# Kernel tuning notes

Measured on AMD Instinct MI355X. Metric: run time of the kernel, lower is better.

The kernel has to match this reference:

```python
import jax, jax.numpy as jnp
import numpy as np

NEG_SLOPE = 0.2
N_NODES = 50000


def _gat_layer(x, src, dst, invalid, W, al, ar, b):
    # x: [N, Fin]; src/dst: [E] (self-loops appended); invalid: [E] bool
    N = x.shape[0]
    H, F = al.shape
    z = (x @ W).reshape(N, H, F)                       # [N,H,F]
    el = jnp.sum(z * al[None], axis=-1)                # [N,H]
    er = jnp.sum(z * ar[None], axis=-1)                # [N,H]
    e = el[src] + er[dst]                              # [E,H]
    e = jnp.where(e > 0, e, NEG_SLOPE * e)             # LeakyReLU(0.2)
    e = jnp.where(invalid[:, None], -jnp.inf, e)       # removed self-loop edges
    # edge softmax per destination node (every node has a self-loop -> max finite)
    m = jax.ops.segment_max(e, dst, num_segments=N)    # [N,H]
    ex = jnp.exp(e - m[dst])
    ex = jnp.where(invalid[:, None], 0.0, ex)
    s = jax.ops.segment_sum(ex, dst, num_segments=N)   # [N,H]
    alpha = ex / s[dst]                                # [E,H]
    msg = z[src] * alpha[:, :, None]                   # [E,H,F]
    out = jax.ops.segment_sum(msg, dst, num_segments=N)  # [N,H,F]
    out = out + b.reshape(1, H, F)
    return jax.nn.elu(out)


def _with_self_loops(src, dst):
    N = N_NODES
    loop = jnp.arange(N, dtype=src.dtype)
    invalid = jnp.concatenate([src == dst, jnp.zeros(N, dtype=bool)])
    return jnp.concatenate([src, loop]), jnp.concatenate([dst, loop]), invalid


def setup_inputs() -> dict:
    key = jax.random.key(0)
    ks = jax.random.split(key, 12)
    N, Fin, H0, F0, H1, C = N_NODES, 256, 4, 32, 1, 40
    E = 800000
    sc = lambda k, shp, fan: jax.random.normal(k, shp, jnp.float32) * (1.0 / np.sqrt(fan))
    return {
        "x": jax.random.normal(ks[0], (N, Fin), jnp.float32),
        "src": jax.random.randint(ks[1], (E,), 0, N, jnp.int32),
        "dst": jax.random.randint(ks[2], (E,), 0, N, jnp.int32),
        "W0": sc(ks[3], (Fin, H0 * F0), Fin),
        "al0": sc(ks[4], (H0, F0), F0),
        "ar0": sc(ks[5], (H0, F0), F0),
        "b0": jnp.zeros((H0 * F0,), jnp.float32),
        "W1": sc(ks[6], (H0 * F0, H1 * C), H0 * F0),
        "al1": sc(ks[7], (H1, C), C),
        "ar1": sc(ks[8], (H1, C), C),
        "b1": jnp.zeros((C,), jnp.float32),
    }


def reference(x, src, dst, W0, al0, ar0, b0, W1, al1, ar1, b1):
    s, d, invalid = _with_self_loops(src, dst)
    h = _gat_layer(x, s, d, invalid, W0, al0, ar0, b0)   # [N,4,32]
    h = h.reshape(h.shape[0], -1)                        # flatten(1) -> [N,128]
    h = _gat_layer(h, s, d, invalid, W1, al1, ar1, b1)   # [N,1,40]
    return h.mean(axis=1)                                # mean over heads -> [N,40]
```

## Files before the change

kernel.cpp:

```cpp
#include <hip/hip_runtime.h>
#include <stdint.h>

#define NN 50000
#define EE 800000
#define CAP 48
#define NXCD 8
#define NPX 6250
#define EPB 2048
#define NCHUNK 391

typedef __bf16 bf16x8 __attribute__((ext_vector_type(8)));
typedef float  f32x4  __attribute__((ext_vector_type(4)));

__device__ __forceinline__ float bflo(unsigned int w){ union{unsigned int i;float f;}c; c.i=w<<16; return c.f; }
__device__ __forceinline__ float bfhi(unsigned int w){ union{unsigned int i;float f;}c; c.i=w&0xFFFF0000u; return c.f; }
__device__ __forceinline__ float bfs(unsigned short u){ union{unsigned int i;float f;}c; c.i=((unsigned int)u)<<16; return c.f; }
__device__ __forceinline__ bf16x8 bf8_zero(){
  bf16x8 v;
  #pragma unroll
  for (int j=0;j<8;++j) v[j]=(__bf16)0.f;
  return v;
}

__global__ __launch_bounds__(256) void k_prepW0(const float* __restrict__ W0,
                                                __bf16* __restrict__ Wg){
  int tg = blockIdx.x*256 + threadIdx.x;
  if (tg >= 4096) return;
  int k8 = tg >> 7, n = tg & 127;
  bf16x8 v;
  #pragma unroll
  for (int j=0;j<8;++j) v[j] = (__bf16)W0[(k8*8+j)*128 + n];
  *(bf16x8*)(Wg + ((size_t)(k8*128 + n))*8) = v;
}

__global__ __launch_bounds__(256) void k_gemm0(const float* __restrict__ x,
    const __bf16* __restrict__ Wg, const float* __restrict__ al0, const float* __restrict__ ar0,
    __bf16* __restrict__ z0b, float* __restrict__ el0, float* __restrict__ er0,
    int* __restrict__ cursor, int* __restrict__ csrv){
  const int tid = threadIdx.x;
  const int wv = tid >> 6, ln = tid & 63, q = ln >> 4, mr = ln & 15;
  const int nhalf = wv & 1, mhalf = wv >> 1;
  const int m0w = blockIdx.x*64 + mhalf*32;
  const int n0w = nhalf*64;
  f32x4 acc[2][4];
  #pragma unroll
  for (int mt=0;mt<2;++mt)
    #pragma unroll
    for (int nt=0;nt<4;++nt) acc[mt][nt] = (f32x4){0.f,0.f,0.f,0.f};
  const bool av0 = (m0w + mr) < NN;
  const bool av1 = (m0w + 16 + mr) < NN;
  const float* xr0 = x + (size_t)(m0w + mr)*256;
  const float* xr1 = x + (size_t)(m0w + 16 + mr)*256;
  #pragma unroll
  for (int kc=0;kc<8;++kc){
    int ko = kc*32 + q*8;
    bf16x8 a0 = bf8_zero(), a1 = bf8_zero();
    if (av0){
      float4 p = *(const float4*)(xr0 + ko);
      float4 p2 = *(const float4*)(xr0 + ko + 4);
      a0[0]=(__bf16)p.x; a0[1]=(__bf16)p.y; a0[2]=(__bf16)p.z; a0[3]=(__bf16)p.w;
      a0[4]=(__bf16)p2.x; a0[5]=(__bf16)p2.y; a0[6]=(__bf16)p2.z; a0[7]=(__bf16)p2.w;
    }
    if (av1){
      float4 p = *(const float4*)(xr1 + ko);
      float4 p2 = *(const float4*)(xr1 + ko + 4);
      a1[0]=(__bf16)p.x; a1[1]=(__bf16)p.y; a1[2]=(__bf16)p.z; a1[3]=(__bf16)p.w;
      a1[4]=(__bf16)p2.x; a1[5]=(__bf16)p2.y; a1[6]=(__bf16)p2.z; a1[7]=(__bf16)p2.w;
    }
    const __bf16* wb = Wg + ((size_t)((kc*4+q)*128 + n0w + mr))*8;
    #pragma unroll
    for (int nt=0;nt<4;++nt){
      bf16x8 bf = *(const bf16x8*)(wb + (size_t)nt*16*8);
      acc[0][nt] = __builtin_amdgcn_mfma_f32_16x16x32_bf16(a0, bf, acc[0][nt], 0,0,0);
      acc[1][nt] = __builtin_amdgcn_mfma_f32_16x16x32_bf16(a1, bf, acc[1][nt], 0,0,0);
    }
  }
  float alv[4], arv[4];
  #pragma unroll
  for (int nt=0;nt<4;++nt){ int c = n0w + nt*16 + mr; alv[nt]=al0[c]; arv[nt]=ar0[c]; }
  #pragma unroll
  for (int mt=0;mt<2;++mt){
    #pragma unroll
    for (int r=0;r<4;++r){
      int grow = m0w + mt*16 + q*4 + r;
      if (grow < NN){
        #pragma unroll
        for (int nt=0;nt<4;++nt)
          z0b[(size_t)grow*128 + n0w + nt*16 + mr] = (__bf16)acc[mt][nt][r];
      }
      float pl0 = acc[mt][0][r]*alv[0] + acc[mt][1][r]*alv[1];
      float pr0 = acc[mt][0][r]*arv[0] + acc[mt][1][r]*arv[1];
      float pl1 = acc[mt][2][r]*alv[2] + acc[mt][3][r]*alv[3];
      float pr1 = acc[mt][2][r]*arv[2] + acc[mt][3][r]*arv[3];
      #pragma unroll
      for (int off=1; off<16; off<<=1){
        pl0 += __shfl_xor(pl0, off, 16); pr0 += __shfl_xor(pr0, off, 16);
        pl1 += __shfl_xor(pl1, off, 16); pr1 += __shfl_xor(pr1, off, 16);
      }
      if (mr==0 && grow<NN){
        el0[grow*4 + 2*nhalf]   = pl0; er0[grow*4 + 2*nhalf]   = pr0;
        el0[grow*4 + 2*nhalf+1] = pl1; er0[grow*4 + 2*nhalf+1] = pr1;
        if (nhalf==0){ csrv[(size_t)grow*CAP] = grow; cursor[grow] = 1; }
      }
    }
  }
}

__global__ __launch_bounds__(256) void k_scatter(const int* __restrict__ src,
    const int* __restrict__ dst, int* __restrict__ cursor, int* __restrict__ csrv){
  const int xcd = blockIdx.x & 7;
  const int chunk = blockIdx.x >> 3;
  const int lo = xcd*NPX, hi = lo + NPX;
  int e = chunk*EPB + threadIdx.x;
  #pragma unroll
  for (int it=0; it<EPB/256; ++it, e += 256){
    if (e < EE){
      int d = dst[e];
      if (d >= lo && d < hi){
        int s = src[e];
        unsigned int inv = (s==d) ? 0x80000000u : 0u;
        int pos = atomicAdd(&cursor[d], 1);
        csrv[(size_t)d*CAP + pos] = (int)((unsigned int)s | inv);
      }
    }
  }
}

__global__ __launch_bounds__(256) void k_wedge0(const int* __restrict__ csrv,
    const int* __restrict__ cursor, const float* __restrict__ el0,
    const float* __restrict__ er0, unsigned short* __restrict__ wt){
  int slot = blockIdx.x*256 + threadIdx.x;
  int node = slot / CAP;
  int si = slot - node*CAP;
  if (si >= cursor[node]) return;
  int v = csrv[slot];
  int u = v & 0x7FFFFFFF;
  float4 ls = *(const float4*)(el0 + (size_t)u*4);
  float4 rd = *(const float4*)(er0 + (size_t)node*4);
  float e0=ls.x+rd.x; e0 = e0>0.f?e0:0.2f*e0;
  float e1=ls.y+rd.y; e1 = e1>0.f?e1:0.2f*e1;
  float e2=ls.z+rd.z; e2 = e2>0.f?e2:0.2f*e2;
  float e3=ls.w+rd.w; e3 = e3>0.f?e3:0.2f*e3;
  bool inv = (v < 0);
  union { __bf16 b[4]; uint2 u2; } pk;
  pk.b[0]=(__bf16)(inv?0.f:__expf(e0)); pk.b[1]=(__bf16)(inv?0.f:__expf(e1));
  pk.b[2]=(__bf16)(inv?0.f:__expf(e2)); pk.b[3]=(__bf16)(inv?0.f:__expf(e3));
  *(uint2*)(wt + (size_t)slot*4) = pk.u2;
}

__global__ __launch_bounds__(256) void k_wedge1(const int* __restrict__ csrv,
    const int* __restrict__ cursor, const float* __restrict__ el1,
    const float* __restrict__ er1, unsigned short* __restrict__ wt1){
  int slot = blockIdx.x*256 + threadIdx.x;
  int node = slot / CAP;
  int si = slot - node*CAP;
  if (si >= cursor[node]) return;
  int v = csrv[slot];
  int u = v & 0x7FFFFFFF;
  float e = el1[u] + er1[node]; e = e>0.f?e:0.2f*e;
  float w = (v<0) ? 0.f : __expf(e);
  union { __bf16 b; unsigned short s; } pk; pk.b = (__bf16)w;
  wt1[slot] = pk.s;
}

__global__ __launch_bounds__(256) void k_agg0(const unsigned short* __restrict__ z0b,
    const unsigned short* __restrict__ wt,
    const int* __restrict__ cursor, const int* __restrict__ csrv,
    const float* __restrict__ b0, unsigned short* __restrict__ hb){
  int lane = threadIdx.x & 63;
  int i = __builtin_amdgcn_readfirstlane(blockIdx.x*4 + (threadIdx.x >> 6));
  int h1 = lane >> 4;
  int lane2 = lane << 1;
  float ax=0.f, ay=0.f, s=0.f;
  int p = i*CAP, pe = p + cursor[i];
  for (; p+8<=pe; p+=8){
    int4 va = *(const int4*)(csrv + p);
    int4 vb = *(const int4*)(csrv + p + 4);
    int v[8] = {va.x,va.y,va.z,va.w,vb.x,vb.y,vb.z,vb.w};
    float w[8];
    #pragma unroll
    for (int j=0;j<8;++j) w[j] = bfs(wt[(size_t)(p+j)*4 + h1]);
    unsigned int zw[8];
    #pragma unroll
    for (int j=0;j<8;++j)
      zw[j] = *(const unsigned int*)(z0b + (size_t)(v[j]&0x7FFFFFFF)*128 + lane2);
    #pragma unroll
    for (int j=0;j<8;++j){
      s += w[j]; ax = fmaf(w[j], bflo(zw[j]), ax); ay = fmaf(w[j], bfhi(zw[j]), ay);
    }
  }
  for (; p+4<=pe; p+=4){
    int4 va = *(const int4*)(csrv + p);
    int v[4] = {va.x,va.y,va.z,va.w};
    float w[4];
    #pragma unroll
    for (int j=0;j<4;++j) w[j] = bfs(wt[(size_t)(p+j)*4 + h1]);
    unsigned int zw[4];
    #pragma unroll
    for (int j=0;j<4;++j)
      zw[j] = *(const unsigned int*)(z0b + (size_t)(v[j]&0x7FFFFFFF)*128 + lane2);
    #pragma unroll
    for (int j=0;j<4;++j){
      s += w[j]; ax = fmaf(w[j], bflo(zw[j]), ax); ay = fmaf(w[j], bfhi(zw[j]), ay);
    }
  }
  for (; p<pe; ++p){
    int u = csrv[p] & 0x7FFFFFFF;
    float w = bfs(wt[(size_t)p*4 + h1]);
    unsigned int zw = *(const unsigned int*)(z0b + (size_t)u*128 + lane2);
    s += w; ax = fmaf(w, bflo(zw), ax); ay = fmaf(w, bfhi(zw), ay);
  }
  float inv = 1.f/s;
  float ox = ax*inv + b0[lane*2], oy = ay*inv + b0[lane*2+1];
  ox = ox>0.f?ox:__expf(ox)-1.f; oy = oy>0.f?oy:__expf(oy)-1.f;
  union { __bf16 b[2]; unsigned int u; } pk;
  pk.b[0]=(__bf16)ox; pk.b[1]=(__bf16)oy;
  *(unsigned int*)(hb + (size_t)i*128 + lane2) = pk.u;
}

__global__ __launch_bounds__(256) void k_gemm1(const __bf16* __restrict__ hb,
    const float* __restrict__ W1, const float* __restrict__ al1, const float* __restrict__ ar1,
    __bf16* __restrict__ z1b, float* __restrict__ el1, float* __restrict__ er1){
  __shared__ __bf16 Blds[16][48][8];
  const int tid = threadIdx.x;
  for (int t=tid; t<16*48*8; t+=256) (&Blds[0][0][0])[t] = (__bf16)0.f;
  __syncthreads();
  for (int t=tid; t<5120; t+=256){
    int k = t/40, n = t - k*40;
    Blds[k>>3][n][k&7] = (__bf16)W1[t];
  }
  __syncthreads();
  const int wm = tid >> 6, ln = tid & 63, q = ln >> 4, mr = ln & 15;
  const int m0 = blockIdx.x*64 + wm*16;
  const int arow = m0 + mr;
  const bool av = (arow < NN);
  f32x4 acc[3];
  #pragma unroll
  for (int nt=0;nt<3;++nt) acc[nt] = (f32x4){0.f,0.f,0.f,0.f};
  #pragma unroll
  for (int kc=0;kc<4;++kc){
    bf16x8 af = bf8_zero();
    if (av) af = *(const bf16x8*)(hb + (size_t)arow*128 + kc*32 + q*8);
    #pragma unroll
    for (int nt=0;nt<3;++nt){
      bf16x8 bf = *(const bf16x8*)&Blds[kc*4+q][nt*16+mr][0];
      acc[nt] = __builtin_amdgcn_mfma_f32_16x16x32_bf16(af, bf, acc[nt], 0,0,0);
    }
  }
  float alv[3], arv[3];
  #pragma unroll
  for (int nt=0;nt<3;++nt){
    int c = nt*16+mr;
    alv[nt] = (c<40) ? al1[c] : 0.f;
    arv[nt] = (c<40) ? ar1[c] : 0.f;
  }
  #pragma unroll
  for (int r=0;r<4;++r){
    int grow = m0 + q*4 + r;
    if (grow < NN){
      #pragma unroll
      for (int nt=0;nt<3;++nt){
        int c = nt*16+mr;
        if (c < 40) z1b[(size_t)grow*40 + c] = (__bf16)acc[nt][r];
      }
    }
    float pl = acc[0][r]*alv[0] + acc[1][r]*alv[1] + acc[2][r]*alv[2];
    float pr = acc[0][r]*arv[0] + acc[1][r]*arv[1] + acc[2][r]*arv[2];
    #pragma unroll
    for (int off=1; off<16; off<<=1){ pl += __shfl_xor(pl, off, 16); pr += __shfl_xor(pr, off, 16); }
    if (mr==0 && grow<NN){ el1[grow]=pl; er1[grow]=pr; }
  }
}

__global__ __launch_bounds__(256) void k_agg1(const unsigned short* __restrict__ z1b,
    const unsigned short* __restrict__ wt1,
    const int* __restrict__ cursor, const int* __restrict__ csrv,
    const float* __restrict__ b1, float* __restrict__ out){
  int lane = threadIdx.x & 63;
  int i = __builtin_amdgcn_readfirstlane(blockIdx.x*4 + (threadIdx.x >> 6));
  int fl = (lane < 20) ? (lane<<1) : 0;
  float ax=0.f, ay=0.f, s=0.f;
  int p = i*CAP, pe = p + cursor[i];
  for (; p+8<=pe; p+=8){
    int4 va = *(const int4*)(csrv + p);
    int4 vb = *(const int4*)(csrv + p + 4);
    int v[8] = {va.x,va.y,va.z,va.w,vb.x,vb.y,vb.z,vb.w};
    uint4 qw = *(const uint4*)(wt1 + p);
    float w[8] = {bflo(qw.x),bfhi(qw.x),bflo(qw.y),bfhi(qw.y),
                  bflo(qw.z),bfhi(qw.z),bflo(qw.w),bfhi(qw.w)};
    unsigned int zw[8];
    #pragma unroll
    for (int j=0;j<8;++j)
      zw[j] = *(const unsigned int*)(z1b + (size_t)(v[j]&0x7FFFFFFF)*40 + fl);
    #pragma unroll
    for (int j=0;j<8;++j){
      s += w[j]; ax = fmaf(w[j], bflo(zw[j]), ax); ay = fmaf(w[j], bfhi(zw[j]), ay);
    }
  }
  for (; p+4<=pe; p+=4){
    int4 va = *(const int4*)(csrv + p);
    int v[4] = {va.x,va.y,va.z,va.w};
    uint2 qw = *(const uint2*)(wt1 + p);
    float w[4] = {bflo(qw.x),bfhi(qw.x),bflo(qw.y),bfhi(qw.y)};
    unsigned int zw[4];
    #pragma unroll
    for (int j=0;j<4;++j)
      zw[j] = *(const unsigned int*)(z1b + (size_t)(v[j]&0x7FFFFFFF)*40 + fl);
    #pragma unroll
    for (int j=0;j<4;++j){
      s += w[j]; ax = fmaf(w[j], bflo(zw[j]), ax); ay = fmaf(w[j], bfhi(zw[j]), ay);
    }
  }
  for (; p<pe; ++p){
    int u = csrv[p] & 0x7FFFFFFF;
    float w = bfs(wt1[p]);
    unsigned int zw = *(const unsigned int*)(z1b + (size_t)u*40 + fl);
    s += w; ax = fmaf(w, bflo(zw), ax); ay = fmaf(w, bfhi(zw), ay);
  }
  if (lane < 20){
    float inv = 1.f/s;
    float ox = ax*inv + b1[lane*2], oy = ay*inv + b1[lane*2+1];
    ox = ox>0.f?ox:__expf(ox)-1.f; oy = oy>0.f?oy:__expf(oy)-1.f;
    *(float2*)(out + (size_t)i*40 + (lane<<1)) = make_float2(ox, oy);
  }
}

extern "C" void kernel_launch(void* const* d_in, const int* in_sizes, int n_in,
                              void* d_out, int out_size, void* d_ws, size_t ws_size,
                              hipStream_t stream){
  const float* x   = (const float*)d_in[0];
  const int*   src = (const int*)d_in[1];
  const int*   dst = (const int*)d_in[2];
  const float* W0  = (const float*)d_in[3];
  const float* al0 = (const float*)d_in[4];
  const float* ar0 = (const float*)d_in[5];
  const float* b0  = (const float*)d_in[6];
  const float* W1  = (const float*)d_in[7];
  const float* al1 = (const float*)d_in[8];
  const float* ar1 = (const float*)d_in[9];
  const float* b1  = (const float*)d_in[10];
  float* out = (float*)d_out;

  __bf16* z0b = (__bf16*)d_ws;
  __bf16* hb  = z0b + (size_t)NN*128;
  __bf16* z1b = hb  + (size_t)NN*128;
  __bf16* Wg  = z1b + (size_t)NN*40;
  unsigned short* wt = (unsigned short*)(Wg + 32768);
  float* el0 = (float*)(wt + (size_t)NN*CAP*4);
  float* er0 = el0 + (size_t)NN*4;
  float* el1 = er0 + (size_t)NN*4;
  float* er1 = el1 + NN;
  int* cursor = (int*)(er1 + NN);
  int* csrv   = cursor + NN;
  unsigned short* wt1 = (unsigned short*)hb;

  k_prepW0 <<<16, 256, 0, stream>>>(W0, Wg);
  k_gemm0<<<(NN+63)/64, 256, 0, stream>>>(x, Wg, al0, ar0, z0b, el0, er0, cursor, csrv);
  k_scatter<<<NCHUNK*NXCD, 256, 0, stream>>>(src, dst, cursor, csrv);
  k_wedge0<<<(NN*CAP)/256, 256, 0, stream>>>(csrv, cursor, el0, er0, wt);
  k_agg0 <<<NN/4, 256, 0, stream>>>((const unsigned short*)z0b, wt, cursor, csrv, b0, (unsigned short*)hb);
  k_gemm1<<<(NN+63)/64, 256, 0, stream>>>(hb, W1, al1, ar1, z1b, el1, er1);
  k_wedge1<<<(NN*CAP)/256, 256, 0, stream>>>(csrv, cursor, el1, er1, wt1);
  k_agg1 <<<NN/4, 256, 0, stream>>>((const unsigned short*)z1b, wt1, cursor, csrv, b1, out);
}
```

Baseline: 248.9 us.

## Replace XCD-filtered scatter with two-pass binning and unroll aggregation by 16

The old scatter had every block read all 800K edges eight times over, once per XCD node-range filter. It now uses a two-pass bucketing scheme. A first kernel bins edges by destination range into eight per-range queues using LDS counters and one global atomic per bin. A second kernel inserts each queue's edges into the CSR, with each block mapped to the XCD that owns that range. This removes the eightfold redundant reading of src/dst, at the cost of an extra queue write and read plus another launch. The aggregation loops in both layers also gain a 16-wide unrolled stage, so more gathers are in flight per iteration, which raises register pressure.

```diff
diff --git a/kernel.cpp b/kernel.cpp
--- a/kernel.cpp
+++ b/kernel.cpp
@@ -6,8 +6,9 @@
 #define CAP 48
 #define NXCD 8
 #define NPX 6250
-#define EPB 2048
-#define NCHUNK 391
+#define QCAP 110592
+#define NBA 391
+#define NBB 432
 
 typedef __bf16 bf16x8 __attribute__((ext_vector_type(8)));
 typedef float  f32x4  __attribute__((ext_vector_type(4)));
@@ -23,14 +24,61 @@
 }
 
 __global__ __launch_bounds__(256) void k_prepW0(const float* __restrict__ W0,
-                                                __bf16* __restrict__ Wg){
+    __bf16* __restrict__ Wg, int* __restrict__ qcur){
   int tg = blockIdx.x*256 + threadIdx.x;
-  if (tg >= 4096) return;
+  if (tg >= 4096){ if (tg < 4104) qcur[tg-4096] = 0; return; }
   int k8 = tg >> 7, n = tg & 127;
   bf16x8 v;
   #pragma unroll
   for (int j=0;j<8;++j) v[j] = (__bf16)W0[(k8*8+j)*128 + n];
   *(bf16x8*)(Wg + ((size_t)(k8*128 + n))*8) = v;
+}
+
+__global__ __launch_bounds__(256) void k_binA(const int* __restrict__ src,
+    const int* __restrict__ dst, int* __restrict__ qcur, int2* __restrict__ queue){
+  __shared__ int lcnt[8];
+  __shared__ int base[8];
+  int t = threadIdx.x;
+  if (t < 8) lcnt[t] = 0;
+  __syncthreads();
+  int e0 = blockIdx.x*2048 + t;
+  int myidx[8], myr[8], mys[8], myd[8];
+  #pragma unroll
+  for (int it=0; it<8; ++it){
+    int e = e0 + it*256;
+    myr[it] = -1;
+    if (e < EE){
+      int s = src[e], d = dst[e];
+      int r = d / NPX;
+      mys[it]=s; myd[it]=d; myr[it]=r;
+      myidx[it] = atomicAdd(&lcnt[r], 1);
+    }
+  }
+  __syncthreads();
+  if (t < 8) base[t] = atomicAdd(&qcur[t], lcnt[t]);
+  __syncthreads();
+  #pragma unroll
+  for (int it=0; it<8; ++it){
+    if (myr[it] >= 0)
+      queue[(size_t)myr[it]*QCAP + base[myr[it]] + myidx[it]] = make_int2(mys[it], myd[it]);
+  }
+}
+
+__global__ __launch_bounds__(256) void k_binB(const int2* __restrict__ queue,
+    const int* __restrict__ qcur, int* __restrict__ cursor, int* __restrict__ csrv){
+  const int r = blockIdx.x & 7;
+  const int chunk = blockIdx.x >> 3;
+  const int len = qcur[r];
+  int idx = chunk*2048 + threadIdx.x;
+  #pragma unroll
+  for (int it=0; it<8; ++it, idx += 256){
+    if (idx < len){
+      int2 sd = queue[(size_t)r*QCAP + idx];
+      unsigned int inv = (sd.x==sd.y) ? 0x80000000u : 0u;
+      int pos = atomicAdd(&cursor[sd.y], 1);
+      csrv[(size_t)sd.y*CAP + pos] = (int)((unsigned int)sd.x | inv);
+    }
+  }
 }
 
 __global__ __launch_bounds__(256) void k_gemm0(const float* __restrict__ x,
@@ -106,26 +154,6 @@
   }
 }
 
-__global__ __launch_bounds__(256) void k_scatter(const int* __restrict__ src,
-    const int* __restrict__ dst, int* __restrict__ cursor, int* __restrict__ csrv){
-  const int xcd = blockIdx.x & 7;
-  const int chunk = blockIdx.x >> 3;
-  const int lo = xcd*NPX, hi = lo + NPX;
-  int e = chunk*EPB + threadIdx.x;
-  #pragma unroll
-  for (int it=0; it<EPB/256; ++it, e += 256){
-    if (e < EE){
-      int d = dst[e];
-      if (d >= lo && d < hi){
-        int s = src[e];
-        unsigned int inv = (s==d) ? 0x80000000u : 0u;
-        int pos = atomicAdd(&cursor[d], 1);
-        csrv[(size_t)d*CAP + pos] = (int)((unsigned int)s | inv);
-      }
-    }
-  }
-}
-
 __global__ __launch_bounds__(256) void k_wedge0(const int* __restrict__ csrv,
     const int* __restrict__ cursor, const float* __restrict__ el0,
     const float* __restrict__ er0, unsigned short* __restrict__ wt){
@@ -173,10 +201,29 @@
   int lane2 = lane << 1;
   float ax=0.f, ay=0.f, s=0.f;
   int p = i*CAP, pe = p + cursor[i];
+  for (; p+16<=pe; p+=16){
+    int4 a0 = *(const int4*)(csrv + p);
+    int4 a1 = *(const int4*)(csrv + p + 4);
+    int4 a2 = *(const int4*)(csrv + p + 8);
+    int4 a3 = *(const int4*)(csrv + p + 12);
+    int v[16] = {a0.x,a0.y,a0.z,a0.w,a1.x,a1.y,a1.z,a1.w,
+                 a2.x,a2.y,a2.z,a2.w,a3.x,a3.y,a3.z,a3.w};
+    float w[16];
+    #pragma unroll
+    for (int j=0;j<16;++j) w[j] = bfs(wt[(size_t)(p+j)*4 + h1]);
+    unsigned int zw[16];
+    #pragma unroll
+    for (int j=0;j<16;++j)
+      zw[j] = *(const unsigned int*)(z0b + (size_t)(v[j]&0x7FFFFFFF)*128 + lane2);
+    #pragma unroll
+    for (int j=0;j<16;++j){
+      s += w[j]; ax = fmaf(w[j], bflo(zw[j]), ax); ay = fmaf(w[j], bfhi(zw[j]), ay);
+    }
+  }
   for (; p+8<=pe; p+=8){
-    int4 va = *(const int4*)(csrv + p);
-    int4 vb = *(const int4*)(csrv + p + 4);
-    int v[8] = {va.x,va.y,va.z,va.w,vb.x,vb.y,vb.z,vb.w};
+    int4 a0 = *(const int4*)(csrv + p);
+    int4 a1 = *(const int4*)(csrv + p + 4);
+    int v[8] = {a0.x,a0.y,a0.z,a0.w,a1.x,a1.y,a1.z,a1.w};
     float w[8];
     #pragma unroll
     for (int j=0;j<8;++j) w[j] = bfs(wt[(size_t)(p+j)*4 + h1]);
@@ -190,8 +237,8 @@
     }
   }
   for (; p+4<=pe; p+=4){
-    int4 va = *(const int4*)(csrv + p);
-    int v[4] = {va.x,va.y,va.z,va.w};
+    int4 a0 = *(const int4*)(csrv + p);
+    int v[4] = {a0.x,a0.y,a0.z,a0.w};
     float w[4];
     #pragma unroll
     for (int j=0;j<4;++j) w[j] = bfs(wt[(size_t)(p+j)*4 + h1]);
@@ -281,10 +328,32 @@
   int fl = (lane < 20) ? (lane<<1) : 0;
   float ax=0.f, ay=0.f, s=0.f;
   int p = i*CAP, pe = p + cursor[i];
+  for (; p+16<=pe; p+=16){
+    int4 a0 = *(const int4*)(csrv + p);
+    int4 a1 = *(const int4*)(csrv + p + 4);
+    int4 a2 = *(const int4*)(csrv + p + 8);
+    int4 a3 = *(const int4*)(csrv + p + 12);
+    int v[16] = {a0.x,a0.y,a0.z,a0.w,a1.x,a1.y,a1.z,a1.w,
+                 a2.x,a2.y,a2.z,a2.w,a3.x,a3.y,a3.z,a3.w};
+    uint4 q0 = *(const uint4*)(wt1 + p);
+    uint4 q1 = *(const uint4*)(wt1 + p + 8);
+    float w[16] = {bflo(q0.x),bfhi(q0.x),bflo(q0.y),bfhi(q0.y),
+                   bflo(q0.z),bfhi(q0.z),bflo(q0.w),bfhi(q0.w),
+                   bflo(q1.x),bfhi(q1.x),bflo(q1.y),bfhi(q1.y),
+                   bflo(q1.z),bfhi(q1.z),bflo(q1.w),bfhi(q1.w)};
+    unsigned int zw[16];
+    #pragma unroll
+    for (int j=0;j<16;++j)
+      zw[j] = *(const unsigned int*)(z1b + (size_t)(v[j]&0x7FFFFFFF)*40 + fl);
+    #pragma unroll
+    for (int j=0;j<16;++j){
+      s += w[j]; ax = fmaf(w[j], bflo(zw[j]), ax); ay = fmaf(w[j], bfhi(zw[j]), ay);
+    }
+  }
   for (; p+8<=pe; p+=8){
-    int4 va = *(const int4*)(csrv + p);
-    int4 vb = *(const int4*)(csrv + p + 4);
-    int v[8] = {va.x,va.y,va.z,va.w,vb.x,vb.y,vb.z,vb.w};
+    int4 a0 = *(const int4*)(csrv + p);
+    int4 a1 = *(const int4*)(csrv + p + 4);
+    int v[8] = {a0.x,a0.y,a0.z,a0.w,a1.x,a1.y,a1.z,a1.w};
     uint4 qw = *(const uint4*)(wt1 + p);
     float w[8] = {bflo(qw.x),bfhi(qw.x),bflo(qw.y),bfhi(qw.y),
                   bflo(qw.z),bfhi(qw.z),bflo(qw.w),bfhi(qw.w)};
@@ -298,8 +367,8 @@
     }
   }
   for (; p+4<=pe; p+=4){
-    int4 va = *(const int4*)(csrv + p);
-    int v[4] = {va.x,va.y,va.z,va.w};
+    int4 a0 = *(const int4*)(csrv + p);
+    int v[4] = {a0.x,a0.y,a0.z,a0.w};
     uint2 qw = *(const uint2*)(wt1 + p);
     float w[4] = {bflo(qw.x),bfhi(qw.x),bflo(qw.y),bfhi(qw.y)};
     unsigned int zw[4];
@@ -352,14 +421,17 @@
   float* er1 = el1 + NN;
   int* cursor = (int*)(er1 + NN);
   int* csrv   = cursor + NN;
+  int* qcur   = csrv + (size_t)NN*CAP;
+  int2* queue = (int2*)(qcur + 8);
   unsigned short* wt1 = (unsigned short*)hb;
 
-  k_prepW0 <<<16, 256, 0, stream>>>(W0, Wg);
-  k_gemm0<<<(NN+63)/64, 256, 0, stream>>>(x, Wg, al0, ar0, z0b, el0, er0, cursor, csrv);
-  k_scatter<<<NCHUNK*NXCD, 256, 0, stream>>>(src, dst, cursor, csrv);
+  k_prepW0<<<17, 256, 0, stream>>>(W0, Wg, qcur);
+  k_binA  <<<NBA, 256, 0, stream>>>(src, dst, qcur, queue);
+  k_gemm0 <<<(NN+63)/64, 256, 0, stream>>>(x, Wg, al0, ar0, z0b, el0, er0, cursor, csrv);
+  k_binB  <<<NBB, 256, 0, stream>>>(queue, qcur, cursor, csrv);
   k_wedge0<<<(NN*CAP)/256, 256, 0, stream>>>(csrv, cursor, el0, er0, wt);
-  k_agg0 <<<NN/4, 256, 0, stream>>>((const unsigned short*)z0b, wt, cursor, csrv, b0, (unsigned short*)hb);
-  k_gemm1<<<(NN+63)/64, 256, 0, stream>>>(hb, W1, al1, ar1, z1b, el1, er1);
+  k_agg0  <<<NN/4, 256, 0, stream>>>((const unsigned short*)z0b, wt, cursor, csrv, b0, (unsigned short*)hb);
+  k_gemm1 <<<(NN+63)/64, 256, 0, stream>>>(hb, W1, al1, ar1, z1b, el1, er1);
   k_wedge1<<<(NN*CAP)/256, 256, 0, stream>>>(csrv, cursor, el1, er1, wt1);
-  k_agg1 <<<NN/4, 256, 0, stream>>>((const unsigned short*)z1b, wt1, cursor, csrv, b1, out);
-}
+  k_agg1  <<<NN/4, 256, 0, stream>>>((const unsigned short*)z1b, wt1, cursor, csrv, b1, out);
+}
```

Result: slower. 255.5 us (+2.7%).
